# Kernel optimization log

Measured on AMD Instinct MI355X. Metric: run time of the kernel, lower is better.

Reference implementation:

```python
import jax, jax.numpy as jnp
import numpy as np
from functools import reduce

Lx, Ly, D, P, CHI = 8, 8, 8, 2, 32
SIGMA = 0.16  # entry scale so the 64-tensor contraction stays O(1)


def _site(peps, xi, yi, s):
    # open-boundary PEPS: dangling lattice-edge bonds have dim 1 (slice of the full tensor)
    u = D if xi < Lx - 1 else 1
    d = D if xi > 0 else 1
    l = D if yi > 0 else 1
    r = D if yi < Ly - 1 else 1
    T = peps[xi, yi, :u, :d, :l, :r, :]          # (u,d,l,r,P)
    return jnp.take(T, s, axis=-1)               # (u,d,l,r), s is traced int


def _compress(ts, chi):
    """MPS compression (cutoff=0, max_bond=chi). ts: list of (l,r,u) tensors."""
    ts = list(ts)
    n = len(ts)
    # left->right canonicalization (thin SVD, no truncation)
    for i in range(n - 1):
        l, r, u = ts[i].shape
        M = ts[i].transpose(0, 2, 1).reshape(l * u, r)
        U, S, Vh = jnp.linalg.svd(M, full_matrices=False)
        k = U.shape[1]
        ts[i] = U.reshape(l, u, k).transpose(0, 2, 1)        # (l,k,u)
        ts[i + 1] = jnp.einsum('kl,lru->kru', S[:, None] * Vh, ts[i + 1])
    # right->left truncating sweep
    for i in range(n - 1, 0, -1):
        l, r, u = ts[i].shape
        M = ts[i].reshape(l, r * u)
        U, S, Vh = jnp.linalg.svd(M, full_matrices=False)
        keep = min(chi, S.shape[0])
        ts[i] = Vh[:keep].reshape(keep, r, u)
        C = U[:, :keep] * S[None, :keep]                      # (l,keep)
        ts[i - 1] = jnp.einsum('amu,mk->aku', ts[i - 1], C)
    return ts


def _absorb_bottom(bmps, row):
    out = []
    for B, A in zip(bmps, row):
        bl, br, _ = B.shape
        u, d, l, r = A.shape
        T = jnp.einsum('xyd,udlr->xlyru', B, A).reshape(bl * l, br * r, u)
        out.append(T)
    return out


def _absorb_top(bmps, row):
    out = []
    for B, A in zip(bmps, row):
        bl, br, _ = B.shape
        u, d, l, r = A.shape
        T = jnp.einsum('xyu,udlr->xlyrd', B, A).reshape(bl * l, br * r, d)
        out.append(T)
    return out


def _amplitude(peps, s):
    A = [[_site(peps, xi, yi, s[xi * Ly + yi]) for yi in range(Ly)] for xi in range(Lx)]
    # boundary MPS from xmin over rows [0, Lx//2-1]
    bot = [A[0][y][:, 0, :, :].transpose(1, 2, 0) for y in range(Ly)]     # (l,r,u)
    for xi in range(1, Lx // 2):
        bot = _compress(_absorb_bottom(bot, A[xi]), CHI)
    # boundary MPS from xmax over rows [Lx//2, Lx-1]
    top = [A[Lx - 1][y][0, :, :, :].transpose(1, 2, 0) for y in range(Ly)]  # (l,r,d)
    for xi in range(Lx - 2, Lx // 2 - 1, -1):
        top = _compress(_absorb_top(top, A[xi]), CHI)
    # zip the two boundary MPSs along the middle bond
    res = jnp.ones((1, 1), dtype=peps.dtype)
    for y in range(Ly):
        E = jnp.einsum('abk,cdk->acbd', bot[y], top[y])
        a, c, b, d = E.shape
        res = res @ E.reshape(a * c, b * d)
    return res[0, 0]


def setup_inputs() -> dict:
    key = jax.random.key(0)
    k1, k2 = jax.random.split(key)
    peps = jax.random.normal(k1, (Lx, Ly, D, D, D, D, P), dtype=jnp.float32) * SIGMA
    x = jax.random.randint(k2, (16, Lx * Ly), 0, P, dtype=jnp.int32)
    return {"x": x, "peps": peps}


def reference(x, peps):
    return jax.vmap(lambda s: _amplitude(peps, s))(x)   # (batch,) amplitudes
```

## Files before the change

### kernel.cpp

```cpp
#include <hip/hip_runtime.h>


__host__ __device__ static inline int imin_(int a,int b){return a<b?a:b;}

static constexpr int SAMP_J = 991296;
static constexpr int O_CUR = 0;
static constexpr int O_NEW = 65536;
static constexpr int O_TF  = 131072;
static constexpr int O_H2F = 393216;
static constexpr int O_MP  = 393216;
static constexpr int O_H   = 458752;
static constexpr int O_S   = 524288;
static constexpr int O_Y   = 589824;
static constexpr int O_Y2  = 606208;
static constexpr int O_C   = 622592;
static constexpr int O_V   = 630784;
static constexpr int O_GSB = 655360;
static constexpr int O_S4  = O_GSB + 266241;

static const int goff[8] = {0,1,4097,69633,135169,200705,266241,331777};

#define LDK 65

__global__ void k_init_row(double* ws, const float* peps, const int* x, int s0){
  int z=blockIdx.z, y=blockIdx.x;
  int side=z&1, samp=z>>1;
  int xi = side?7:0;
  double* base = ws + (size_t)z*SAMP_J;
  double* cur = base + O_CUR + y*8192;
  int spin = x[(s0+samp)*64 + xi*8 + y];
  const float* pb = peps + (size_t)xi*65536 + (size_t)y*8192 + spin;
  int rd=(y<7)?8:1, ld=(y>0)?8:1;
  int ntot = ld*rd*8;
  for(int e=threadIdx.x; e<ntot; e+=blockDim.x){
    int u=e&7; int r=(e>>3)%rd; int l=e/(8*rd);
    float v = side ? pb[u*128 + l*16 + r*2] : pb[u*1024 + l*16 + r*2];
    cur[e]=(double)v;
  }
  if(y==0 && threadIdx.x==0) base[O_GSB]=1.0;
}

__global__ __launch_bounds__(256)
void k_absorb(double* ws, const float* peps, const int* x, int s0,
              int xi_b, int xi_t, int y, int bl, int brdim){
  int z=blockIdx.z, yb=blockIdx.x;
  int side=z&1, samp=z>>1;
  int xi = side? xi_t : xi_b;
  int so = side? 128:1024, sc = side? 1024:128;
  double* base=ws+(size_t)z*SAMP_J;
  const double* B=base+O_CUR+y*8192;
  float* T=(float*)(base+O_TF);
  int spin=x[(s0+samp)*64+xi*8+y];
  const float* A=peps+(size_t)xi*65536+(size_t)y*8192+spin;
  int Lp=(y>0)?8:1, Rp=(y<7)?8:1;
  int rraw=brdim*Rp;
  __shared__ float As[4096];
  __shared__ double Bs[256];
  int nA=64*Lp*Rp;
  for(int e=threadIdx.x;e<nA;e+=256){
    int rp=e%Rp; int t=e/Rp; int lp=t%Lp; t/=Lp; int p=t&7; int u=t>>3;
    As[e]=A[u*so+p*sc+lp*16+rp*2];
  }
  for(int e=threadIdx.x;e<bl*8;e+=256)
    Bs[e]=B[((e>>3)*brdim+yb)*8+(e&7)];
  __syncthreads();
  int ntot=bl*Lp*Rp*8;
  for(int e=threadIdx.x;e<ntot;e+=256){
    int u=e&7; int t=e>>3; int rp=t%Rp; t/=Rp; int lp=t%Lp; int xx=t/Lp;
    double acc=0.0;
    #pragma unroll
    for(int p=0;p<8;p++) acc+=Bs[xx*8+p]*(double)As[((u*8+p)*Lp+lp)*Rp+rp];
    T[(size_t)((xx*Lp+lp)*rraw + yb*Rp+rp)*8 + u]=(float)acc;
  }
}

__global__ void k_mmGT(double* ws, int Aoff, int Boff, int Coff, int ni, int nk, int nj){
  double* base=ws+(size_t)blockIdx.z*SAMP_J;
  const double* A=base+Aoff;
  const float* B=(const float*)(base+Boff);
  float* C=(float*)(base+Coff);
  __shared__ double As[16][17]; __shared__ float Bs[16][17];
  int tx=threadIdx.x, ty=threadIdx.y;
  int i0=blockIdx.x*16, j0=blockIdx.y*16;
  double acc=0.0;
  for(int k0=0;k0<nk;k0+=16){
    As[ty][tx]=(i0+ty<ni && k0+tx<nk)? A[(size_t)(i0+ty)*nk + k0+tx] : 0.0;
    Bs[ty][tx]=(k0+ty<nk && j0+tx<nj)? B[(size_t)(k0+ty)*nj + j0+tx] : 0.f;
    __syncthreads();
    #pragma unroll
    for(int t=0;t<16;t++) acc+=As[ty][t]*(double)Bs[t][tx];
    __syncthreads();
  }
  if(i0+ty<ni && j0+tx<nj) C[(size_t)(i0+ty)*nj + j0+tx]=(float)acc;
}

__global__ void k_mm(double* ws, int Aoff, int Boff, int Coff, int ni, int nk, int nj){
  double* base=ws+(size_t)blockIdx.z*SAMP_J;
  const double* A=base+Aoff; const double* B=base+Boff; double* C=base+Coff;
  __shared__ double As[16][17], Bs[16][17];
  int tx=threadIdx.x, ty=threadIdx.y;
  int i0=blockIdx.x*16, j0=blockIdx.y*16;
  double acc=0.0;
  for(int k0=0;k0<nk;k0+=16){
    As[ty][tx]=(i0+ty<ni && k0+tx<nk)? A[(size_t)(i0+ty)*nk + k0+tx] : 0.0;
    Bs[ty][tx]=(k0+ty<nk && j0+tx<nj)? B[(size_t)(k0+ty)*nj + j0+tx] : 0.0;
    __syncthreads();
    #pragma unroll
    for(int t=0;t<16;t++) acc+=As[ty][t]*Bs[t][tx];
    __syncthreads();
  }
  if(i0+ty<ni && j0+tx<nj) C[(size_t)(i0+ty)*nj + j0+tx]=acc;
}
__global__ void k_mm_tn(double* ws, int Aoff, int Boff, int Coff, int ni, int nk, int nj){
  double* base=ws+(size_t)blockIdx.z*SAMP_J;
  const double* A=base+Aoff; const double* B=base+Boff; double* C=base+Coff;
  __shared__ double As[16][17], Bs[16][17];
  int tx=threadIdx.x, ty=threadIdx.y;
  int i0=blockIdx.x*16, j0=blockIdx.y*16;
  double acc=0.0;
  for(int k0=0;k0<nk;k0+=16){
    As[ty][tx]=(k0+ty<nk && i0+tx<ni)? A[(size_t)(k0+ty)*ni + i0+tx] : 0.0;
    Bs[ty][tx]=(k0+ty<nk && j0+tx<nj)? B[(size_t)(k0+ty)*nj + j0+tx] : 0.0;
    __syncthreads();
    #pragma unroll
    for(int t=0;t<16;t++) acc+=As[t][ty]*Bs[t][tx];
    __syncthreads();
  }
  if(i0+ty<ni && j0+tx<nj) C[(size_t)(i0+ty)*nj + j0+tx]=acc;
}

__global__ void k_gacc2(double* ws, int H2off, int Toff, int Goff, int ldim, int rdim){
  int bx=blockIdx.x, by=blockIdx.y;
  if(by<bx) return;
  double* base=ws+(size_t)blockIdx.z*SAMP_J;
  const float* H2=(const float*)(base+H2off);
  const float* T=(const float*)(base+Toff);
  double* G=base+Goff;
  __shared__ float As[16][17], Bs[16][17];
  int tx=threadIdx.x, ty=threadIdx.y;
  int r0=bx*16, r1=by*16;
  double acc=0.0;
  int ktot=ldim*8;
  for(int k0=0;k0<ktot;k0+=16){
    int kk=k0+ty; int l2=kk>>3; int u=kk&7;
    As[ty][tx]=(kk<ktot)? H2[((size_t)l2*rdim + r0+tx)*8 + u] : 0.f;
    Bs[ty][tx]=(kk<ktot)? T [((size_t)l2*rdim + r1+tx)*8 + u] : 0.f;
    __syncthreads();
    #pragma unroll
    for(int t=0;t<16;t++) acc+=(double)As[t][ty]*(double)Bs[t][tx];
    __syncthreads();
  }
  G[(size_t)(r0+ty)*rdim + r1+tx]=acc;
  if(by>bx) G[(size_t)(r1+tx)*rdim + r0+ty]=acc;
}

__global__ void k_gscale(double* ws, int Goff, int n){
  int tid=threadIdx.x;
  double* base=ws+(size_t)blockIdx.z*SAMP_J;
  double* G=base+Goff;
  __shared__ double red[256]; __shared__ double s_sc;
  double mx=0.0;
  for(int i=tid;i<n;i+=256) mx=fmax(mx,fabs(G[(size_t)i*n+i]));
  red[tid]=mx; __syncthreads();
  for(int w=128;w>0;w>>=1){ if(tid<w) red[tid]=fmax(red[tid],red[tid+w]); __syncthreads(); }
  if(tid==0) s_sc=(red[0]>0.0)?1.0/red[0]:1.0;
  __syncthreads();
  double sc=s_sc;
  for(int e=tid;e<n*n;e+=256) G[e]*=sc;
}

__global__ __launch_bounds__(256)
void k_mp(double* ws, int Toff, int Coff, int Moff, int rraw, int keep){
  int li=blockIdx.x, tid=threadIdx.x;
  double* base=ws+(size_t)blockIdx.z*SAMP_J;
  const float* T=(const float*)(base+Toff) + (size_t)li*rraw*8;
  const double* Cc=base+Coff;
  double* M=base+Moff+(size_t)li*keep*8;
  __shared__ float Ts[2048];
  for(int e=tid;e<rraw*8;e+=256) Ts[e]=T[e];
  __syncthreads();
  for(int e=tid;e<keep*8;e+=256){
    int u=e&7, k=e>>3;
    double acc=0.0;
    for(int r=0;r<rraw;r++) acc+=(double)Ts[r*8+u]*Cc[(size_t)r*keep+k];
    M[k*8+u]=acc;
  }
}

__global__ void k_t2mp(double* ws, int n){
  double* base=ws+(size_t)blockIdx.z*SAMP_J;
  const float* T=(const float*)(base+O_TF);
  for(int e=blockIdx.x*blockDim.x+threadIdx.x;e<n;e+=gridDim.x*blockDim.x)
    base[O_MP+e]=(double)T[e];
}

__device__ void dev_jacobi(double* K, float* W, int q, int tid, int sweeps,
                           double* csC, double* csS, int* csP, int* csQ){
  int NT=blockDim.x;
  int m=q-1, npairs=q>>1;
  int L=NT/npairs;
  int inv2=(m+1)>>1;
  for(int sweep=0;sweep<sweeps;sweep++)
  for(int rnd=0;rnd<m;rnd++){
    if(tid<npairs){
      int i0=(int)(((long long)rnd*(long long)inv2)%m);
      int p,qq;
      if(tid==0){ p=i0; qq=q-1; }
      else {
        p=i0+tid; if(p>=m) p-=m;
        qq=i0-tid; if(qq<0) qq+=m;
      }
      if(p>qq){int t=p;p=qq;qq=t;}
      double c=1.0,s2=0.0;
      double apq=K[p*LDK+qq];
      double app=K[p*LDK+p], aqq=K[qq*LDK+qq];
      if(fabs(apq) > 1e-18*(fabs(app)+fabs(aqq))+1e-300){
        double tau=(aqq-app)/(2.0*apq);
        double t=(tau>=0.0?1.0:-1.0)/(fabs(tau)+sqrt(1.0+tau*tau));
        c=1.0/sqrt(1.0+t*t); s2=t*c;
      }
      csP[tid]=p; csQ[tid]=qq; csC[tid]=c; csS[tid]=s2;
    }
    __syncthreads();
    int pr=tid/L, lane=tid%L;
    {
      int p=csP[pr], qq=csQ[pr];
      double c=csC[pr], s2=csS[pr];
      for(int j=lane;j<q;j+=L){
        double kp=K[p*LDK+j], kq=K[qq*LDK+j];
        K[p*LDK+j]=c*kp-s2*kq; K[qq*LDK+j]=s2*kp+c*kq;
      }
    }
    __syncthreads();
    {
      int p=csP[pr], qq=csQ[pr];
      double c=csC[pr], s2=csS[pr];
      float cf=(float)c, sf=(float)s2;
      for(int j=lane;j<q;j+=L){
        double kp=K[j*LDK+p], kq=K[j*LDK+qq];
        K[j*LDK+p]=c*kp-s2*kq; K[j*LDK+qq]=s2*kp+c*kq;
        float wp=W[j*LDK+p], wq=W[j*LDK+qq];
        W[j*LDK+p]=cf*wp-sf*wq; W[j*LDK+qq]=sf*wp+cf*wq;
      }
    }
    __syncthreads();
  }
}

__device__ void dev_select(const double* K, int q, int keep, int tid,
                           double* evals, int* idxs){
  for(int a=tid;a<q;a+=blockDim.x) evals[a]=K[a*LDK+a];
  __syncthreads();
  if(tid<64){
    int a=tid;
    double v=(a<q)? evals[a] : -1.0e300;
    for(int j=0;j<keep;j++){
      double bv=v; int bi=a;
      for(int off=1;off<64;off<<=1){
        double ov=__shfl_xor(bv,off); int oi=__shfl_xor(bi,off);
        if(ov>bv || (ov==bv && oi<bi)){ bv=ov; bi=oi; }
      }
      if(a==bi) v=-1.0e300;
      if(tid==0) idxs[j]=bi;
    }
  }
  __syncthreads();
}

__device__ void dev_orthV(double* V, int n, int keep, double* red){
  int tid=threadIdx.x;
  for(int j=0;j<keep;j++){
    double vj=(tid<n)? V[(size_t)tid*keep+j] : 0.0;
    for(int pass=0;pass<2;pass++){
      for(int t=0;t<j;t++){
        double vt=(tid<n)? V[(size_t)tid*keep+t] : 0.0;
        double p=vj*vt;
        for(int off=1;off<64;off<<=1) p+=__shfl_xor(p,off);
        if((tid&63)==0) red[tid>>6]=p;
        __syncthreads();
        double d=red[0]+red[1]+red[2]+red[3];
        vj-=d*vt;
        __syncthreads();
      }
    }
    double p=vj*vj;
    for(int off=1;off<64;off<<=1) p+=__shfl_xor(p,off);
    if((tid&63)==0) red[tid>>6]=p;
    __syncthreads();
    double nrm=red[0]+red[1]+red[2]+red[3];
    vj=vj/sqrt(fmax(nrm,1e-300));
    if(tid<n) V[(size_t)tid*keep+j]=vj;
    __syncthreads();
  }
}

__global__ __launch_bounds__(256)
void k_eig_direct(double* ws, int Soff, int MPoff, int l, int ru, int keep,
                  int newoff, int Coff){
  int tid=threadIdx.x;
  double* base=ws+(size_t)blockIdx.z*SAMP_J;
  const double* S=base+Soff;
  const double* MP=base+MPoff;
  double* C=base+Coff;
  double* NM=base+newoff;
  double* V=base+O_V;
  __shared__ double K[64*LDK];
  __shared__ float W[64*LDK];
  __shared__ double csC[32], csS[32];
  __shared__ int csP[32], csQ[32];
  __shared__ double evals[64]; __shared__ int idxs[64];
  __shared__ double red[4];
  int q=ru;
  for(int e=tid;e<q*q;e+=256){
    int a=e/q,b=e%q;
    K[a*LDK+b]=0.5*(S[(size_t)a*q+b]+S[(size_t)b*q+a]);
    W[a*LDK+b]=(a==b)?1.f:0.f;
  }
  __syncthreads();
  dev_jacobi(K,W,q,tid,8,csC,csS,csP,csQ);
  dev_select(K,q,keep,tid,evals,idxs);
  for(int e=tid;e<ru*keep;e+=256){
    int col=e/keep, j=e%keep;
    V[e]=(double)W[col*LDK+idxs[j]];
  }
  __syncthreads();
  dev_orthV(V,ru,keep,red);
  for(int e=tid;e<keep*ru;e+=256){
    int j=e/ru, col=e%ru;
    NM[e]=V[(size_t)col*keep+j];
  }
  for(int e=tid;e<l*keep;e+=256){
    int i=e/keep, j=e%keep;
    const double* Mi=MP+(size_t)i*ru;
    double acc=0.0;
    for(int c=0;c<ru;c++) acc+=Mi[c]*V[(size_t)c*keep+j];
    C[e]=acc;
  }
}

__device__ void dev_smul(const double* A, const double* Yin, double* Yout,
                         double* Yt, int tid){
  double acc[32];
  int i=tid&255, j0=(tid>>8)*32;
  #pragma unroll
  for(int j=0;j<32;j++) acc[j]=0.0;
  for(int cb=0;cb<16;cb++){
    __syncthreads();
    for(int e=tid;e<1024;e+=512) Yt[e]=Yin[cb*1024+e];
    __syncthreads();
    const double* Arow=A+(size_t)i*256+cb*16;
    for(int c=0;c<16;c++){
      double sv=Arow[c];
      const double* Yr=Yt+c*64+j0;
      #pragma unroll
      for(int j=0;j<32;j++) acc[j]+=sv*Yr[j];
    }
  }
  #pragma unroll
  for(int j=0;j<32;j++) Yout[(size_t)i*64+j0+j]=acc[j];
  __syncthreads();
}

__device__ void dev_cholqr(double* Yg, int ncols, double* Kd, double* Yt,
                           double* Ri, double* shv, int tid){
  int rpb=1024/ncols, nblk=256/rpb, n2=ncols*ncols;
  for(int e=tid;e<n2;e+=512) Kd[(e/ncols)*LDK+(e%ncols)]=0.0;
  for(int b=0;b<nblk;b++){
    __syncthreads();
    for(int e=tid;e<1024;e+=512) Yt[e]=Yg[b*1024+e];
    __syncthreads();
    for(int e=tid;e<n2;e+=512){
      int a=e/ncols, c=e%ncols;
      if(c>=a){
        double acc=0.0;
        for(int r=0;r<rpb;r++) acc+=Yt[r*ncols+a]*Yt[r*ncols+c];
        Kd[a*LDK+c]+=acc;
      }
    }
  }
  __syncthreads();
  if(tid==0){
    double tr=0.0;
    for(int j=0;j<ncols;j++) tr+=Kd[j*LDK+j];
    shv[0]=(tr/ncols)*1e-14+1e-290;
  }
  __syncthreads();
  double lam=shv[0];
  for(int i=tid;i<ncols;i+=512) Kd[i*LDK+i]+=lam;
  __syncthreads();
  for(int j=0;j<ncols;j++){
    double d=Kd[j*LDK+j];
    if(!(d>lam*0.25)) d=lam*0.25;
    double invd=1.0/d;
    if(tid==0) Kd[j*LDK+j]=d;
    int w=ncols-1-j;
    for(int e=tid;e<w*w;e+=512){
      int i2=j+1+e/w, k2=j+1+e%w;
      if(k2>=i2) Kd[i2*LDK+k2]-=Kd[j*LDK+i2]*Kd[j*LDK+k2]*invd;
    }
    __syncthreads();
  }
  for(int i=tid;i<ncols;i+=512) Yt[i]=1.0/sqrt(Kd[i*LDK+i]);
  __syncthreads();
  for(int e=tid;e<n2;e+=512){
    int i=e/ncols, k=e%ncols;
    if(k>=i) Kd[i*LDK+k]*=Yt[i];
  }
  __syncthreads();
  if(tid<ncols){
    int j=tid;
    Ri[j*66+j]=1.0/Kd[j*LDK+j];
    for(int i=j-1;i>=0;i--){
      double s=0.0;
      for(int k=i+1;k<=j;k++) s+=Kd[i*LDK+k]*Ri[k*66+j];
      Ri[i*66+j]=-s/Kd[i*LDK+i];
    }
  }
  __syncthreads();
  {
    int j=tid%ncols, rg=tid/ncols;
    for(int b=0;b<nblk;b++){
      for(int e=tid;e<1024;e+=512) Yt[e]=Yg[b*1024+e];
      __syncthreads();
      double xr[2];
      #pragma unroll
      for(int r4=0;r4<2;r4++){
        int r=rg*2+r4;
        double acc=0.0;
        for(int k=0;k<=j;k++) acc+=Yt[r*ncols+k]*Ri[k*66+j];
        xr[r4]=acc;
      }
      __syncthreads();
      #pragma unroll
      for(int r4=0;r4<2;r4++){
        int r=rg*2+r4;
        Yg[(size_t)b*1024 + r*ncols + j]=xr[r4];
      }
    }
  }
  __syncthreads();
}

__global__ __launch_bounds__(512,1)
void k_eig_sub(double* ws, int Soff, int S4off, int MPoff, int l, int keep,
               int newoff, int Coff){
  const int RU=256;
  int tid=threadIdx.x;
  double* base=ws+(size_t)blockIdx.z*SAMP_J;
  const double* S =base+Soff;
  const double* S4=base+S4off;
  const double* MP=base+MPoff;
  double* Ya=base+O_Y;
  double* Yb=base+O_Y2;
  double* V =base+O_V;
  double* C =base+Coff;
  double* NM=base+newoff;
  __shared__ double Kd[64*LDK];
  __shared__ double Ri[64*66];
  __shared__ float  Wf[64*LDK];
  __shared__ double Yt[1024];
  __shared__ double red[516];
  __shared__ unsigned long long om[256];
  __shared__ double csC[32], csS[32];
  __shared__ int csP[32], csQ[32];
  __shared__ double evals[64]; __shared__ int idxs[64];

  for(int c2=tid;c2<256;c2+=512){
    unsigned long long mask=0ull;
    for(int j=0;j<64;j++){
      unsigned h=(unsigned)(c2*1103515245u)^(unsigned)((j+1)*2654435761u);
      h^=h>>13; h*=0x9E3779B1u;
      mask |= ((unsigned long long)((h>>16)&1u))<<j;
    }
    om[c2]=mask;
  }
  __syncthreads();

  for(int e=tid;e<RU*64;e+=512){
    int i=e>>6, j=e&63;
    const double* Si=S4+(size_t)i*RU;
    double acc=0.0;
    for(int c2=0;c2<RU;c2++)
      acc += ((om[c2]>>j)&1ull)? Si[c2] : -Si[c2];
    Ya[e]=acc;
  }
  __syncthreads();
  dev_cholqr(Ya,64,Kd,Yt,Ri,red+512,tid);
  dev_cholqr(Ya,64,Kd,Yt,Ri,red+512,tid);
  for(int it=0;it<4;it++){
    dev_smul(S4,Ya,Yb,Yt,tid);
    double* t=Ya; Ya=Yb; Yb=t;
    dev_cholqr(Ya,64,Kd,Yt,Ri,red+512,tid);
  }
  dev_cholqr(Ya,64,Kd,Yt,Ri,red+512,tid);
  dev_smul(S,Ya,Yb,Yt,tid);

  for(int e=tid;e<4096;e+=512){ int a=e>>6,c=e&63; Kd[a*LDK+c]=0.0; }
  for(int b=0;b<32;b++){
    __syncthreads();
    { int e=tid; Yt[e]=Ya[b*512+e]; }
    { int e=tid; Yt[512+e]=Yb[b*512+e]; }
    __syncthreads();
    for(int i=0;i<8;i++){
      int idx=tid*8+i; int a=idx>>6, c=idx&63;
      double acc=Kd[a*LDK+c];
      for(int r=0;r<8;r++) acc+=Yt[r*64+a]*Yt[512+r*64+c];
      Kd[a*LDK+c]=acc;
    }
  }
  __syncthreads();
  for(int e=tid;e<4096;e+=512){
    int a=e>>6,c=e&63;
    if(a<c){ double m=0.5*(Kd[a*LDK+c]+Kd[c*LDK+a]); Kd[a*LDK+c]=m; Kd[c*LDK+a]=m; }
  }
  __syncthreads();
  for(int e=tid;e<4096;e+=512){ int a=e>>6,c=e&63; Wf[a*LDK+c]=(a==c)?1.f:0.f; }
  __syncthreads();
  dev_jacobi(Kd,Wf,64,tid,6,csC,csS,csP,csQ);
  dev_select(Kd,64,keep,tid,evals,idxs);
  for(int e=tid;e<RU*keep;e+=512){
    int i=e/keep, j=e%keep; int vj=idxs[j];
    const double* Yr=Ya+(size_t)i*64;
    double acc=0.0;
    for(int t=0;t<64;t++) acc+=Yr[t]*(double)Wf[t*LDK+vj];
    V[e]=acc;
  }
  __syncthreads();
  dev_cholqr(V,keep,Kd,Yt,Ri,red+512,tid);
  for(int e=tid;e<keep*RU;e+=512){
    int j=e/RU, col=e%RU;
    NM[e]=V[(size_t)col*keep+j];
  }
  for(int e=tid;e<l*keep;e+=512){
    int i=e/keep, j=e%keep;
    const double* Mi=MP+(size_t)i*RU;
    double acc=0.0;
    for(int col=0;col<RU;col++) acc+=Mi[col]*V[(size_t)col*keep+j];
    C[e]=acc;
  }
}

__global__ void k_copy(double* ws){
  double* base=ws+(size_t)blockIdx.z*SAMP_J;
  for(int e=blockIdx.x*blockDim.x+threadIdx.x;e<65536;e+=gridDim.x*blockDim.x)
    base[O_CUR+e]=base[O_NEW+e];
}

__global__ __launch_bounds__(256)
void k_final(double* ws, float* out, int s0){
  int z=blockIdx.z, tid=threadIdx.x;
  const double* bot=ws+(size_t)(2*z)*SAMP_J+O_CUR;
  const double* top=ws+(size_t)(2*z+1)*SAMP_J+O_CUR;
  __shared__ double v[1024], v2[1024];
  __shared__ float w[8192];
  const int Bf[9]={1,8,32,32,32,32,32,8,1};
  if(tid==0) v[0]=1.0;
  __syncthreads();
  for(int y=0;y<8;y++){
    int a=Bf[y], b=Bf[y+1];
    const double* By=bot+y*8192;
    const double* Ty=top+y*8192;
    for(int e=tid;e<a*b*8;e+=256){
      int k2=e&7; int bb=(e>>3)%b; int cc=e/(8*b);
      double acc=0.0;
      for(int aa=0;aa<a;aa++) acc+=v[aa*a+cc]*By[(aa*b+bb)*8+k2];
      w[(cc*b+bb)*8+k2]=(float)acc;
    }
    __syncthreads();
    for(int e=tid;e<b*b;e+=256){
      int dd=e%b; int bb=e/b;
      double acc=0.0;
      for(int cc=0;cc<a;cc++)
        for(int k2=0;k2<8;k2++)
          acc+=(double)w[(cc*b+bb)*8+k2]*Ty[(cc*b+dd)*8+k2];
      v2[bb*b+dd]=acc;
    }
    __syncthreads();
    for(int e=tid;e<b*b;e+=256) v[e]=v2[e];
    __syncthreads();
  }
  if(tid==0) out[s0+z]=(float)v[0];
}

static void run_compress_dual(double* ws, const float* peps, const int* x,
                              int s0, int ns, int xib, int xit, bool first,
                              hipStream_t stream){
  int njobs=2*ns;
  int Bin[9]; Bin[0]=1; Bin[8]=1;
  for(int i=1;i<8;i++) Bin[i]= first?8:((i==1||i==7)?8:32);
  int lraw[8], rraw[8];
  for(int y=0;y<8;y++){ lraw[y]=Bin[y]*((y>0)?8:1); rraw[y]=Bin[y+1]*((y<7)?8:1); }
  int kch[8];
  { int kp=1;
    for(int y=0;y<8;y++){ int n=(y<7)?Bin[y+1]*8:1; kch[y]=imin_(kp*8,n); kp=kch[y]; } }
  int keep[8];
  keep[7]=imin_(32, imin_(kch[6], 8));
  for(int y=6;y>=1;y--) keep[y]=imin_(32, imin_(kch[y-1], keep[y+1]*8));

  for(int y=0;y<7;y++){
    k_absorb<<<dim3(Bin[y+1],1,njobs),256,0,stream>>>(ws,peps,x,s0,xib,xit,y,Bin[y],Bin[y+1]);
    int l=lraw[y], r8=rraw[y]*8;
    k_mmGT<<<dim3((l+15)/16,(r8+15)/16,njobs),dim3(16,16),0,stream>>>(
        ws,O_GSB+goff[y],O_TF,O_H2F,l,l,r8);
    k_gacc2<<<dim3(rraw[y]/16,rraw[y]/16,njobs),dim3(16,16),0,stream>>>(
        ws,O_H2F,O_TF,O_GSB+goff[y+1],l,rraw[y]);
    k_gscale<<<dim3(1,1,njobs),256,0,stream>>>(ws,O_GSB+goff[y+1],rraw[y]);
  }
  for(int y=7;y>=1;y--){
    k_absorb<<<dim3(Bin[y+1],1,njobs),256,0,stream>>>(ws,peps,x,s0,xib,xit,y,Bin[y],Bin[y+1]);
    int ru=(y==7)?8:keep[y+1]*8;
    if(y==7) k_t2mp<<<dim3(2,1,njobs),256,0,stream>>>(ws,lraw[7]*8);
    else     k_mp<<<dim3(lraw[y],1,njobs),256,0,stream>>>(ws,O_TF,O_C,O_MP,rraw[y],keep[y+1]);
    int l=lraw[y];
    k_mm<<<dim3((l+15)/16,(ru+15)/16,njobs),dim3(16,16),0,stream>>>(
        ws,O_GSB+goff[y],O_MP,O_H,l,l,ru);
    k_mm_tn<<<dim3((ru+15)/16,(ru+15)/16,njobs),dim3(16,16),0,stream>>>(
        ws,O_MP,O_H,O_S,ru,l,ru);
    if(ru<=64){
      k_eig_direct<<<dim3(1,1,njobs),256,0,stream>>>(ws,O_S,O_MP,l,ru,keep[y],
                    O_NEW+y*8192,O_C);
    } else {
      k_mm<<<dim3(16,16,njobs),dim3(16,16),0,stream>>>(ws,O_S,O_S,O_H,256,256,256);
      k_mm<<<dim3(16,16,njobs),dim3(16,16),0,stream>>>(ws,O_H,O_H,O_S4,256,256,256);
      k_eig_sub<<<dim3(1,1,njobs),512,0,stream>>>(ws,O_S,O_S4,O_MP,l,keep[y],
                    O_NEW+y*8192,O_C);
    }
  }
  k_absorb<<<dim3(Bin[1],1,njobs),256,0,stream>>>(ws,peps,x,s0,xib,xit,0,1,Bin[1]);
  k_mp<<<dim3(1,1,njobs),256,0,stream>>>(ws,O_TF,O_C,O_NEW+0,rraw[0],keep[1]);
  k_copy<<<dim3(32,1,njobs),256,0,stream>>>(ws);
}

extern "C" void kernel_launch(void* const* d_in, const int* in_sizes, int n_in,
                              void* d_out, int out_size, void* d_ws, size_t ws_size,
                              hipStream_t stream){
  const int*   x    = (const int*)d_in[0];
  const float* peps = (const float*)d_in[1];
  float* out = (float*)d_out;
  double* ws = (double*)d_ws;
  size_t samp_bytes = (size_t)2*SAMP_J*sizeof(double);
  int max_chunk=(int)(ws_size/samp_bytes);
  if(max_chunk<1) max_chunk=1;
  if(max_chunk>16) max_chunk=16;
  for(int s0=0;s0<16;s0+=max_chunk){
    int ns=imin_(max_chunk,16-s0);
    int njobs=2*ns;
    k_init_row<<<dim3(8,1,njobs),64,0,stream>>>(ws,peps,x,s0);
    run_compress_dual(ws,peps,x,s0,ns,1,6,true ,stream);
    run_compress_dual(ws,peps,x,s0,ns,2,5,false,stream);
    run_compress_dual(ws,peps,x,s0,ns,3,4,false,stream);
    k_final<<<dim3(1,1,ns),256,0,stream>>>(ws,out,s0);
  }
}
```

Baseline: 91.08 ms.

## Cut barriers in Jacobi, Cholesky QR and subspace products via larger tiles

Each thread group in the Jacobi eigensolver now computes its own rotation redundantly, so the shared-memory rotation table and one barrier per round go away. Cholesky QR's factorisation, triangular inverse and trace now run inside a single 64-lane wavefront using shuffles and compiler memory fences, replacing a block-wide barrier per column. The subspace products and Gram accumulation stage 4096-element tiles instead of 1024, cutting the number of barrier-separated passes. The cost is more shared memory and a serial per-lane Cholesky loop, which relies on lockstep wavefront execution for correctness.

New measurement: 94.30 ms. 1.04x slower.

```diff
diff --git a/kernel.cpp b/kernel.cpp
--- a/kernel.cpp
+++ b/kernel.cpp
@@ -21,6 +21,7 @@
 static const int goff[8] = {0,1,4097,69633,135169,200705,266241,331777};
 
 #define LDK 65
+#define WMEMF() __asm__ volatile("" ::: "memory")
 
 __global__ void k_init_row(double* ws, const float* peps, const int* x, int s0){
   int z=blockIdx.z, y=blockIdx.x;
@@ -194,47 +195,36 @@
     base[O_MP+e]=(double)T[e];
 }
 
-__device__ void dev_jacobi(double* K, float* W, int q, int tid, int sweeps,
-                           double* csC, double* csS, int* csP, int* csQ){
+__device__ void dev_jacobi(double* K, float* W, int q, int tid, int sweeps){
   int NT=blockDim.x;
   int m=q-1, npairs=q>>1;
   int L=NT/npairs;
   int inv2=(m+1)>>1;
+  int pr=tid/L, lane=tid%L;
   for(int sweep=0;sweep<sweeps;sweep++)
   for(int rnd=0;rnd<m;rnd++){
-    if(tid<npairs){
-      int i0=(int)(((long long)rnd*(long long)inv2)%m);
-      int p,qq;
-      if(tid==0){ p=i0; qq=q-1; }
-      else {
-        p=i0+tid; if(p>=m) p-=m;
-        qq=i0-tid; if(qq<0) qq+=m;
-      }
-      if(p>qq){int t=p;p=qq;qq=t;}
-      double c=1.0,s2=0.0;
-      double apq=K[p*LDK+qq];
-      double app=K[p*LDK+p], aqq=K[qq*LDK+qq];
-      if(fabs(apq) > 1e-18*(fabs(app)+fabs(aqq))+1e-300){
-        double tau=(aqq-app)/(2.0*apq);
-        double t=(tau>=0.0?1.0:-1.0)/(fabs(tau)+sqrt(1.0+tau*tau));
-        c=1.0/sqrt(1.0+t*t); s2=t*c;
-      }
-      csP[tid]=p; csQ[tid]=qq; csC[tid]=c; csS[tid]=s2;
-    }
-    __syncthreads();
-    int pr=tid/L, lane=tid%L;
+    int i0=(int)(((long long)rnd*(long long)inv2)%m);
+    int p,qq;
+    if(pr==0){ p=i0; qq=q-1; }
+    else {
+      p=i0+pr; if(p>=m) p-=m;
+      qq=i0-pr; if(qq<0) qq+=m;
+    }
+    if(p>qq){int t=p;p=qq;qq=t;}
+    double c=1.0,s2=0.0;
+    double apq=K[p*LDK+qq];
+    double app=K[p*LDK+p], aqq=K[qq*LDK+qq];
+    if(fabs(apq) > 1e-18*(fabs(app)+fabs(aqq))+1e-300){
+      double tau=(aqq-app)/(2.0*apq);
+      double t=(tau>=0.0?1.0:-1.0)/(fabs(tau)+sqrt(1.0+tau*tau));
+      c=1.0/sqrt(1.0+t*t); s2=t*c;
+    }
+    for(int j=lane;j<q;j+=L){
+      double kp=K[p*LDK+j], kq=K[qq*LDK+j];
+      K[p*LDK+j]=c*kp-s2*kq; K[qq*LDK+j]=s2*kp+c*kq;
+    }
+    __syncthreads();
     {
-      int p=csP[pr], qq=csQ[pr];
-      double c=csC[pr], s2=csS[pr];
-      for(int j=lane;j<q;j+=L){
-        double kp=K[p*LDK+j], kq=K[qq*LDK+j];
-        K[p*LDK+j]=c*kp-s2*kq; K[qq*LDK+j]=s2*kp+c*kq;
-      }
-    }
-    __syncthreads();
-    {
-      int p=csP[pr], qq=csQ[pr];
-      double c=csC[pr], s2=csS[pr];
       float cf=(float)c, sf=(float)s2;
       for(int j=lane;j<q;j+=L){
         double kp=K[j*LDK+p], kq=K[j*LDK+qq];
@@ -306,8 +296,6 @@
   double* V=base+O_V;
   __shared__ double K[64*LDK];
   __shared__ float W[64*LDK];
-  __shared__ double csC[32], csS[32];
-  __shared__ int csP[32], csQ[32];
   __shared__ double evals[64]; __shared__ int idxs[64];
   __shared__ double red[4];
   int q=ru;
@@ -317,7 +305,7 @@
     W[a*LDK+b]=(a==b)?1.f:0.f;
   }
   __syncthreads();
-  dev_jacobi(K,W,q,tid,8,csC,csS,csP,csQ);
+  dev_jacobi(K,W,q,tid,8);
   dev_select(K,q,keep,tid,evals,idxs);
   for(int e=tid;e<ru*keep;e+=256){
     int col=e/keep, j=e%keep;
@@ -344,12 +332,12 @@
   int i=tid&255, j0=(tid>>8)*32;
   #pragma unroll
   for(int j=0;j<32;j++) acc[j]=0.0;
-  for(int cb=0;cb<16;cb++){
-    __syncthreads();
-    for(int e=tid;e<1024;e+=512) Yt[e]=Yin[cb*1024+e];
-    __syncthreads();
-    const double* Arow=A+(size_t)i*256+cb*16;
-    for(int c=0;c<16;c++){
+  for(int cb=0;cb<4;cb++){
+    __syncthreads();
+    for(int e=tid;e<4096;e+=512) Yt[e]=Yin[cb*4096+e];
+    __syncthreads();
+    const double* Arow=A+(size_t)i*256+cb*64;
+    for(int c=0;c<64;c++){
       double sv=Arow[c];
       const double* Yr=Yt+c*64+j0;
       #pragma unroll
@@ -362,79 +350,78 @@
 }
 
 __device__ void dev_cholqr(double* Yg, int ncols, double* Kd, double* Yt,
-                           double* Ri, double* shv, int tid){
-  int rpb=1024/ncols, nblk=256/rpb, n2=ncols*ncols;
+                           double* Ri, int tid){
+  int rowsb=4096/ncols; if(rowsb>256) rowsb=256;
+  int nblk=256/rowsb;
+  int n2=ncols*ncols;
   for(int e=tid;e<n2;e+=512) Kd[(e/ncols)*LDK+(e%ncols)]=0.0;
   for(int b=0;b<nblk;b++){
     __syncthreads();
-    for(int e=tid;e<1024;e+=512) Yt[e]=Yg[b*1024+e];
+    for(int e=tid;e<rowsb*ncols;e+=512) Yt[e]=Yg[(size_t)b*rowsb*ncols+e];
     __syncthreads();
     for(int e=tid;e<n2;e+=512){
-      int a=e/ncols, c=e%ncols;
-      if(c>=a){
+      int a=e/ncols, cc=e%ncols;
+      if(cc>=a){
         double acc=0.0;
-        for(int r=0;r<rpb;r++) acc+=Yt[r*ncols+a]*Yt[r*ncols+c];
-        Kd[a*LDK+c]+=acc;
-      }
-    }
-  }
-  __syncthreads();
-  if(tid==0){
-    double tr=0.0;
-    for(int j=0;j<ncols;j++) tr+=Kd[j*LDK+j];
-    shv[0]=(tr/ncols)*1e-14+1e-290;
-  }
-  __syncthreads();
-  double lam=shv[0];
-  for(int i=tid;i<ncols;i+=512) Kd[i*LDK+i]+=lam;
-  __syncthreads();
-  for(int j=0;j<ncols;j++){
-    double d=Kd[j*LDK+j];
-    if(!(d>lam*0.25)) d=lam*0.25;
-    double invd=1.0/d;
-    if(tid==0) Kd[j*LDK+j]=d;
-    int w=ncols-1-j;
-    for(int e=tid;e<w*w;e+=512){
-      int i2=j+1+e/w, k2=j+1+e%w;
-      if(k2>=i2) Kd[i2*LDK+k2]-=Kd[j*LDK+i2]*Kd[j*LDK+k2]*invd;
-    }
-    __syncthreads();
-  }
-  for(int i=tid;i<ncols;i+=512) Yt[i]=1.0/sqrt(Kd[i*LDK+i]);
-  __syncthreads();
-  for(int e=tid;e<n2;e+=512){
-    int i=e/ncols, k=e%ncols;
-    if(k>=i) Kd[i*LDK+k]*=Yt[i];
-  }
-  __syncthreads();
-  if(tid<ncols){
-    int j=tid;
-    Ri[j*66+j]=1.0/Kd[j*LDK+j];
-    for(int i=j-1;i>=0;i--){
-      double s=0.0;
-      for(int k=i+1;k<=j;k++) s+=Kd[i*LDK+k]*Ri[k*66+j];
-      Ri[i*66+j]=-s/Kd[i*LDK+i];
+        for(int r=0;r<rowsb;r++) acc+=Yt[r*ncols+a]*Yt[r*ncols+cc];
+        Kd[a*LDK+cc]+=acc;
+      }
+    }
+  }
+  __syncthreads();
+  if(tid<64){
+    int k=tid;
+    double dv=(k<ncols)? Kd[k*LDK+k] : 0.0;
+    double tr=dv;
+    for(int off=1;off<64;off<<=1) tr+=__shfl_xor(tr,off);
+    double lam=(tr/ncols)*1e-14+1e-290;
+    if(k<ncols){
+      Kd[k*LDK+k]=dv+lam;
+      WMEMF();
+      for(int j=0;j<ncols;j++){
+        double d=Kd[j*LDK+j];
+        if(!(d>lam*0.25)) d=lam*0.25;
+        if(k==j) Kd[j*LDK+j]=d;
+        if(k>j){
+          double invd=1.0/d;
+          double kjk=Kd[j*LDK+k];
+          for(int i=j+1;i<=k;i++)
+            Kd[i*LDK+k]-=Kd[j*LDK+i]*kjk*invd;
+        }
+        WMEMF();
+      }
+      double dk=Kd[k*LDK+k];
+      Yt[k]=1.0/sqrt(dk);
+      WMEMF();
+      for(int i=0;i<k;i++) Kd[i*LDK+k]*=Yt[i];
+      Kd[k*LDK+k]=dk*Yt[k];
+      WMEMF();
+      Ri[k*66+k]=1.0/Kd[k*LDK+k];
+      for(int i=k-1;i>=0;i--){
+        double s=0.0;
+        for(int kk=i+1;kk<=k;kk++) s+=Kd[i*LDK+kk]*Ri[kk*66+k];
+        Ri[i*66+k]=-s/Kd[i*LDK+i];
+      }
     }
   }
   __syncthreads();
   {
     int j=tid%ncols, rg=tid/ncols;
+    int rpt=(rowsb*ncols)/512;
     for(int b=0;b<nblk;b++){
-      for(int e=tid;e<1024;e+=512) Yt[e]=Yg[b*1024+e];
+      for(int e=tid;e<rowsb*ncols;e+=512) Yt[e]=Yg[(size_t)b*rowsb*ncols+e];
       __syncthreads();
-      double xr[2];
-      #pragma unroll
-      for(int r4=0;r4<2;r4++){
-        int r=rg*2+r4;
+      double xr[8];
+      for(int r4=0;r4<rpt;r4++){
+        int r=rg*rpt+r4;
         double acc=0.0;
-        for(int k=0;k<=j;k++) acc+=Yt[r*ncols+k]*Ri[k*66+j];
+        for(int kk=0;kk<=j;kk++) acc+=Yt[r*ncols+kk]*Ri[kk*66+j];
         xr[r4]=acc;
       }
       __syncthreads();
-      #pragma unroll
-      for(int r4=0;r4<2;r4++){
-        int r=rg*2+r4;
-        Yg[(size_t)b*1024 + r*ncols + j]=xr[r4];
+      for(int r4=0;r4<rpt;r4++){
+        int r=rg*rpt+r4;
+        Yg[(size_t)b*rowsb*ncols + r*ncols + j]=xr[r4];
       }
     }
   }
@@ -458,11 +445,8 @@
   __shared__ double Kd[64*LDK];
   __shared__ double Ri[64*66];
   __shared__ float  Wf[64*LDK];
-  __shared__ double Yt[1024];
-  __shared__ double red[516];
+  __shared__ double Yt[4096];
   __shared__ unsigned long long om[256];
-  __shared__ double csC[32], csS[32];
-  __shared__ int csP[32], csQ[32];
   __shared__ double evals[64]; __shared__ int idxs[64];
 
   for(int c2=tid;c2<256;c2+=512){
@@ -485,26 +469,25 @@
     Ya[e]=acc;
   }
   __syncthreads();
-  dev_cholqr(Ya,64,Kd,Yt,Ri,red+512,tid);
-  dev_cholqr(Ya,64,Kd,Yt,Ri,red+512,tid);
+  dev_cholqr(Ya,64,Kd,Yt,Ri,tid);
+  dev_cholqr(Ya,64,Kd,Yt,Ri,tid);
   for(int it=0;it<4;it++){
     dev_smul(S4,Ya,Yb,Yt,tid);
     double* t=Ya; Ya=Yb; Yb=t;
-    dev_cholqr(Ya,64,Kd,Yt,Ri,red+512,tid);
-  }
-  dev_cholqr(Ya,64,Kd,Yt,Ri,red+512,tid);
+    dev_cholqr(Ya,64,Kd,Yt,Ri,tid);
+  }
+  dev_cholqr(Ya,64,Kd,Yt,Ri,tid);
   dev_smul(S,Ya,Yb,Yt,tid);
 
   for(int e=tid;e<4096;e+=512){ int a=e>>6,c=e&63; Kd[a*LDK+c]=0.0; }
-  for(int b=0;b<32;b++){
-    __syncthreads();
-    { int e=tid; Yt[e]=Ya[b*512+e]; }
-    { int e=tid; Yt[512+e]=Yb[b*512+e]; }
-    __syncthreads();
-    for(int i=0;i<8;i++){
-      int idx=tid*8+i; int a=idx>>6, c=idx&63;
+  for(int b=0;b<8;b++){
+    __syncthreads();
+    for(int e=tid;e<2048;e+=512){ Yt[e]=Ya[b*2048+e]; Yt[2048+e]=Yb[b*2048+e]; }
+    __syncthreads();
+    for(int e=tid;e<4096;e+=512){
+      int a=e>>6, c=e&63;
       double acc=Kd[a*LDK+c];
-      for(int r=0;r<8;r++) acc+=Yt[r*64+a]*Yt[512+r*64+c];
+      for(int r=0;r<32;r++) acc+=Yt[r*64+a]*Yt[2048+r*64+c];
       Kd[a*LDK+c]=acc;
     }
   }
@@ -516,7 +499,7 @@
   __syncthreads();
   for(int e=tid;e<4096;e+=512){ int a=e>>6,c=e&63; Wf[a*LDK+c]=(a==c)?1.f:0.f; }
   __syncthreads();
-  dev_jacobi(Kd,Wf,64,tid,6,csC,csS,csP,csQ);
+  dev_jacobi(Kd,Wf,64,tid,6);
   dev_select(Kd,64,keep,tid,evals,idxs);
   for(int e=tid;e<RU*keep;e+=512){
     int i=e/keep, j=e%keep; int vj=idxs[j];
@@ -526,7 +509,7 @@
     V[e]=acc;
   }
   __syncthreads();
-  dev_cholqr(V,keep,Kd,Yt,Ri,red+512,tid);
+  dev_cholqr(V,keep,Kd,Yt,Ri,tid);
   for(int e=tid;e<keep*RU;e+=512){
     int j=e/RU, col=e%RU;
     NM[e]=V[(size_t)col*keep+j];
```
